# Performance work log

Hardware: AMD Instinct MI355X
Metric: run time of the kernel (lower is better)

## Reference

```python
import jax, jax.numpy as jnp
import numpy as np

DIM = 512
CHUNK = 64
LN_EPS = 1e-5


def setup_inputs() -> dict:
    key = jax.random.key(0)
    ks = jax.random.split(key, 9)
    B, S, D = 4, 4096, DIM
    x = jax.random.normal(ks[0], (B, S, D), dtype=jnp.float32)
    # Linear weights stored as [in, out] (equivalent to torch W.T)
    W_omega = jax.random.normal(ks[1], (D, D), dtype=jnp.float32) / np.sqrt(D)
    b_omega = jnp.zeros((D,), dtype=jnp.float32)
    log_scale = jnp.full((D,), np.log(0.1), dtype=jnp.float32)
    ln_gamma = jnp.ones((4 * D,), dtype=jnp.float32)
    ln_beta = jnp.zeros((4 * D,), dtype=jnp.float32)
    W1 = jax.random.normal(ks[2], (4 * D, 2 * D), dtype=jnp.float32) / np.sqrt(4 * D)
    b1 = jnp.zeros((2 * D,), dtype=jnp.float32)
    W2 = jax.random.normal(ks[3], (2 * D, D), dtype=jnp.float32) / np.sqrt(2 * D)
    b2 = jnp.zeros((D,), dtype=jnp.float32)
    return {"x": x, "W_omega": W_omega, "b_omega": b_omega, "log_scale": log_scale,
            "ln_gamma": ln_gamma, "ln_beta": ln_beta, "W1": W1, "b1": b1, "W2": W2, "b2": b2}


def reference(x, W_omega, b_omega, log_scale, ln_gamma, ln_beta, W1, b1, W2, b2):
    B, S, D = x.shape
    C = CHUNK
    # S chosen as multiple of C, so pad_len == 0 (matches torch no-pad branch)
    N = S // C
    omega = x @ W_omega + b_omega                      # [B,S,D]
    oc = omega.reshape(B, N, C, D)
    xc = x.reshape(B, N, C, D)
    pos = jnp.arange(1, C + 1, dtype=x.dtype)          # [C]
    pos_scale = (1.0 / jnp.sqrt(pos))[None, None, :, None]
    scale = jnp.exp(log_scale)
    phi = jnp.cumsum(oc * scale * pos_scale, axis=2)   # [B,N,C,D]
    cos_phi = jnp.cos(phi)
    sin_phi = jnp.sin(phi)
    cr = xc * cos_phi                                   # content modulated real
    ci = xc * sin_phi                                   # content modulated imag
    pos_norm = pos[None, None, :, None]
    mr = jnp.cumsum(cr, axis=2) / pos_norm              # memory real
    mi = jnp.cumsum(ci, axis=2) / pos_norm              # memory imag
    rr = mr * cos_phi + mi * sin_phi                    # retrieved real
    ri = mi * cos_phi - mr * sin_phi                    # retrieved imag
    ctx = jnp.concatenate([cr.reshape(B, S, D), ci.reshape(B, S, D),
                           rr.reshape(B, S, D), ri.reshape(B, S, D)], axis=-1)  # [B,S,4D]
    mu = jnp.mean(ctx, axis=-1, keepdims=True)
    var = jnp.mean((ctx - mu) ** 2, axis=-1, keepdims=True)
    h = (ctx - mu) / jnp.sqrt(var + LN_EPS) * ln_gamma + ln_beta
    h = h @ W1 + b1
    h = jax.nn.gelu(h, approximate=False)               # torch GELU default = exact erf
    out = h @ W2 + b2                                   # dropout is identity at eval
    return x + out
```

## Files before the change

### kernel.cpp

```cpp
#include <hip/hip_runtime.h>
#include <hip/hip_bf16.h>
#include <math.h>


typedef __bf16 bf16x8 __attribute__((ext_vector_type(8)));
typedef __bf16 bf16x4 __attribute__((ext_vector_type(4)));
typedef __bf16 bf16x2 __attribute__((ext_vector_type(2)));
typedef float  f32x4  __attribute__((ext_vector_type(4)));

typedef __attribute__((address_space(1))) void* gas_ptr;
typedef __attribute__((address_space(3))) void* las_ptr;

__device__ __forceinline__ void load_lds16(const void* g, void* l) {
    __builtin_amdgcn_global_load_lds((gas_ptr)g, (las_ptr)l, 16, 0, 0);
}

__device__ __forceinline__ void transpose_tile(const float* __restrict__ in,
                                               __bf16* __restrict__ out,
                                               int K, int N, int bx, int by,
                                               float (*tile)[33])
{
    const int tid = threadIdx.x;
    const int tx = tid & 31, ty = tid >> 5;
    const int n0 = bx * 32, k0 = by * 32;
    #pragma unroll
    for (int i = 0; i < 32; i += 8)
        tile[ty + i][tx] = in[(size_t)(k0 + ty + i) * N + n0 + tx];
    __syncthreads();
    #pragma unroll
    for (int i = 0; i < 32; i += 8)
        out[(size_t)(n0 + ty + i) * K + k0 + tx] = (__bf16)tile[tx][ty + i];
}

__global__ __launch_bounds__(256)
void prep_kernel(const float* __restrict__ x, __bf16* __restrict__ xb,
                 const float* __restrict__ W_omega, __bf16* __restrict__ womT,
                 const float* __restrict__ W1, __bf16* __restrict__ w1T,
                 const float* __restrict__ W2, __bf16* __restrict__ w2T)
{
    __shared__ float tile[32][33];
    const int bid = blockIdx.x;
    if (bid < 8192) {
        int i = bid * 256 + threadIdx.x;
        float4 v = ((const float4*)x)[i];
        bf16x4 o = { (__bf16)v.x, (__bf16)v.y, (__bf16)v.z, (__bf16)v.w };
        ((bf16x4*)xb)[i] = o;
    } else if (bid < 8448) {
        int t = bid - 8192;
        transpose_tile(W_omega, womT, 512, 512, t & 15, t >> 4, tile);
    } else if (bid < 10496) {
        int t = bid - 8448;
        transpose_tile(W1, w1T, 2048, 1024, t & 31, t >> 5, tile);
    } else {
        int t = bid - 10496;
        transpose_tile(W2, w2T, 1024, 512, t & 15, t >> 4, tile);
    }
}

template<int MODE>
__global__ __launch_bounds__(256)
void gemm_kernel(const __bf16* __restrict__ A, const __bf16* __restrict__ Bt,
                 const float* __restrict__ bias, const __bf16* __restrict__ resid,
                 void* __restrict__ out, int M, int N, int K)
{
    __shared__ __bf16 As[2][128 * 64];
    __shared__ __bf16 Bs[2][128 * 64];

    const int tid     = threadIdx.x;
    const int tiles_n = N >> 7;
    const int ln_tn   = __ffs(tiles_n) - 1;
    const int per_m   = (M >> 7) >> 3;

    const int xcd = blockIdx.x & 7;
    const int j   = blockIdx.x >> 3;
    const int tile_m = (xcd * per_m + (j >> ln_tn)) << 7;
    const int tile_n = (j & (tiles_n - 1)) << 7;

    const int wave = tid >> 6;
    const int lane = tid & 63;

    const int srow = lane >> 3;
    const int scol = ((lane & 7) ^ srow) << 3;

    const __bf16* Ags = A  + (size_t)(tile_m + wave * 32 + srow) * K + scol;
    const __bf16* Bgs = Bt + (size_t)(tile_n + wave * 32 + srow) * K + scol;

    const int m0 = (wave >> 1) << 6;
    const int n0 = (wave & 1) << 6;
    const int lr = lane & 15;
    const int q  = lane >> 4;
    const int l7 = lane & 7;
    const int fc0 = ((0 + q) ^ l7) << 3;
    const int fc1 = ((4 + q) ^ l7) << 3;

    f32x4 acc[4][4];
    #pragma unroll
    for (int i = 0; i < 4; ++i)
        #pragma unroll
        for (int jj = 0; jj < 4; ++jj)
            acc[i][jj] = (f32x4){0.f, 0.f, 0.f, 0.f};

    const int nIter = K >> 6;

    #pragma unroll
    for (int c = 0; c < 4; ++c) {
        load_lds16(Ags + (size_t)(c * 8) * K, &As[0][(wave * 32 + c * 8) * 64]);
        load_lds16(Bgs + (size_t)(c * 8) * K, &Bs[0][(wave * 32 + c * 8) * 64]);
    }

    for (int it = 0; it < nIter; ++it) {
        const int cur = it & 1;
        __syncthreads();
        if (it + 1 < nIter) {
            const int nk = (it + 1) << 6;
            #pragma unroll
            for (int c = 0; c < 4; ++c) {
                load_lds16(Ags + nk + (size_t)(c * 8) * K, &As[cur ^ 1][(wave * 32 + c * 8) * 64]);
                load_lds16(Bgs + nk + (size_t)(c * 8) * K, &Bs[cur ^ 1][(wave * 32 + c * 8) * 64]);
            }
        }

        const __bf16* as = As[cur];
        const __bf16* bs = Bs[cur];
        {
            bf16x8 af[4], bq[4];
            #pragma unroll
            for (int i = 0; i < 4; ++i)
                af[i] = *(const bf16x8*)&as[(m0 + i * 16 + lr) * 64 + fc0];
            #pragma unroll
            for (int jj = 0; jj < 4; ++jj)
                bq[jj] = *(const bf16x8*)&bs[(n0 + jj * 16 + lr) * 64 + fc0];
            #pragma unroll
            for (int i = 0; i < 4; ++i)
                #pragma unroll
                for (int jj = 0; jj < 4; ++jj)
                    acc[i][jj] = __builtin_amdgcn_mfma_f32_16x16x32_bf16(af[i], bq[jj], acc[i][jj], 0, 0, 0);
        }
        {
            bf16x8 af[4], bq[4];
            #pragma unroll
            for (int i = 0; i < 4; ++i)
                af[i] = *(const bf16x8*)&as[(m0 + i * 16 + lr) * 64 + fc1];
            #pragma unroll
            for (int jj = 0; jj < 4; ++jj)
                bq[jj] = *(const bf16x8*)&bs[(n0 + jj * 16 + lr) * 64 + fc1];
            #pragma unroll
            for (int i = 0; i < 4; ++i)
                #pragma unroll
                for (int jj = 0; jj < 4; ++jj)
                    acc[i][jj] = __builtin_amdgcn_mfma_f32_16x16x32_bf16(af[i], bq[jj], acc[i][jj], 0, 0, 0);
        }
    }

    const int orow0 = tile_m + m0 + (q << 2);
    const int ocol0 = tile_n + n0 + lr;
    #pragma unroll
    for (int i = 0; i < 4; ++i) {
        #pragma unroll
        for (int jj = 0; jj < 4; ++jj) {
            const int col = ocol0 + jj * 16;
            const float bv = bias[col];
            #pragma unroll
            for (int r = 0; r < 4; ++r) {
                const int row = orow0 + i * 16 + r;
                float v = acc[i][jj][r] + bv;
                size_t idx = (size_t)row * N + col;
                if (MODE == 0) {
                    ((__bf16*)out)[idx] = (__bf16)v;
                } else if (MODE == 1) {
                    float g = 0.5f * v * (1.0f + erff(v * 0.70710678118654752f));
                    ((__bf16*)out)[idx] = (__bf16)g;
                } else {
                    ((float*)out)[idx] = v + (float)resid[idx];
                }
            }
        }
    }
}

template<int MODE>
__global__ __launch_bounds__(512, 1)
void gemm256_kernel(const __bf16* __restrict__ A, const __bf16* __restrict__ Bt,
                    const float* __restrict__ bias, void* __restrict__ out,
                    int M, int N, int K)
{
    __shared__ __bf16 As[4][256 * 32];
    __shared__ __bf16 Bs[4][256 * 32];

    const int tid  = threadIdx.x;
    const int wv   = tid >> 6;
    const int lane = tid & 63;
    const int wm   = wv >> 2;
    const int wn   = wv & 3;

    const int tiles_n = N >> 8;
    const int ln_tn   = __ffs(tiles_n) - 1;
    const int per_m   = (M >> 8) >> 3;

    const int xcd = blockIdx.x & 7;
    const int j   = blockIdx.x >> 3;
    const int tile_m = (xcd * per_m + (j >> ln_tn)) << 8;
    const int tile_n = (j & (tiles_n - 1)) << 8;

    const int srow = 16 * wv + (lane >> 2);
    const int sig8 = (((lane & 3) ^ ((lane >> 3) & 3)) << 3);

    const __bf16* Ag = A  + (size_t)(tile_m + srow) * K + sig8;
    const __bf16* Bg = Bt + (size_t)(tile_n + srow) * K + sig8;
    const size_t rowK128 = (size_t)128 * K;
    const int lbase = wv * 512;

    const int lr    = lane & 15;
    const int q4    = lane >> 4;
    const int fslot = ((q4 ^ ((lane >> 1) & 3)) << 3);
    const int arow0 = wm * 128 + lr;
    const int brow0 = wn * 64 + lr;

    const unsigned ldsA0 = (unsigned)(size_t)(las_ptr)&As[0][0];
    const unsigned ldsB0 = (unsigned)(size_t)(las_ptr)&Bs[0][0];
    const unsigned asA = ldsA0 + (unsigned)((arow0 * 32 + fslot) << 1);
    const unsigned asB = ldsB0 + (unsigned)((brow0 * 32 + fslot) << 1);

    f32x4 acc[8][4];
    #pragma unroll
    for (int i = 0; i < 8; ++i)
        #pragma unroll
        for (int jj = 0; jj < 4; ++jj)
            acc[i][jj] = (f32x4){0.f, 0.f, 0.f, 0.f};

    const int NKS = K >> 5;

    auto stage = [&](int ks) {
        const int slot = ks & 3;
        const __bf16* ag = Ag + (ks << 5);
        const __bf16* bg = Bg + (ks << 5);
        load_lds16(ag,           &As[slot][lbase]);
        load_lds16(ag + rowK128, &As[slot][4096 + lbase]);
        load_lds16(bg,           &Bs[slot][lbase]);
        load_lds16(bg + rowK128, &Bs[slot][4096 + lbase]);
    };

    bf16x8 afA[8], bqA[4], afB[8], bqB[4];

#define DSR(d, a, o) asm volatile("ds_read_b128 %0, %1 offset:" o \
                                  : "=v"(d) : "v"(a))
#define SB __builtin_amdgcn_sched_barrier(0)
#define MM4(CAF, CBQ, I)                                                      \
    acc[I][0] = __builtin_amdgcn_mfma_f32_16x16x32_bf16(CAF[I], CBQ[0], acc[I][0], 0, 0, 0); \
    acc[I][1] = __builtin_amdgcn_mfma_f32_16x16x32_bf16(CAF[I], CBQ[1], acc[I][1], 0, 0, 0); \
    acc[I][2] = __builtin_amdgcn_mfma_f32_16x16x32_bf16(CAF[I], CBQ[2], acc[I][2], 0, 0, 0); \
    acc[I][3] = __builtin_amdgcn_mfma_f32_16x16x32_bf16(CAF[I], CBQ[3], acc[I][3], 0, 0, 0);

#define G256_READ(KS, NAF, NBQ)                                               \
    {                                                                         \
        const unsigned aA_ = asA + (unsigned)(((KS) & 3) << 14);              \
        const unsigned aB_ = asB + (unsigned)(((KS) & 3) << 14);              \
        DSR(NAF[0], aA_, "0");    DSR(NAF[1], aA_, "1024");                   \
        DSR(NAF[2], aA_, "2048"); DSR(NAF[3], aA_, "3072");                   \
        DSR(NAF[4], aA_, "4096"); DSR(NAF[5], aA_, "5120");                   \
        DSR(NAF[6], aA_, "6144"); DSR(NAF[7], aA_, "7168");                   \
        DSR(NBQ[0], aB_, "0");    DSR(NBQ[1], aB_, "1024");                   \
        DSR(NBQ[2], aB_, "2048"); DSR(NBQ[3], aB_, "3072");                   \
    }

#define G256_PHASE_FULL(KS, CAF, CBQ, NAF, NBQ)                               \
    {                                                                         \
        const int ks_ = (KS);                                                 \
        asm volatile("s_waitcnt vmcnt(8)" ::: "memory");                      \
        __builtin_amdgcn_s_barrier();                                         \
        asm volatile("" ::: "memory");                                        \
        const int slot_ = (ks_ + 4) & 3;                                      \
        const __bf16* ag_ = Ag + ((ks_ + 4) << 5);                            \
        const __bf16* bg_ = Bg + ((ks_ + 4) << 5);                            \
        const unsigned aA_ = asA + (unsigned)(((ks_ + 1) & 3) << 14);         \
        const unsigned aB_ = asB + (unsigned)(((ks_ + 1) & 3) << 14);         \
        __builtin_amdgcn_s_setprio(1);                                        \
        load_lds16(ag_,           &As[slot_][lbase]);                         \
        MM4(CAF, CBQ, 0) SB;                                                  \
        load_lds16(ag_ + rowK128, &As[slot_][4096 + lbase]);                  \
        MM4(CAF, CBQ, 1) SB;                                                  \
        load_lds16(bg_,           &Bs[slot_][lbase]);                         \
        MM4(CAF, CBQ, 2) SB;                                                  \
        load_lds16(bg_ + rowK128, &Bs[slot_][4096 + lbase]);                  \
        MM4(CAF, CBQ, 3) SB;                                                  \
        DSR(NAF[0], aA_, "0"); DSR(NAF[1], aA_, "1024");                      \
        DSR(NAF[2], aA_, "2048");                                             \
        MM4(CAF, CBQ, 4) SB;                                                  \
        DSR(NAF[3], aA_, "3072"); DSR(NAF[4], aA_, "4096");                   \
        DSR(NAF[5], aA_, "5120");                                             \
        MM4(CAF, CBQ, 5) SB;                                                  \
        DSR(NAF[6], aA_, "6144"); DSR(NAF[7], aA_, "7168");                   \
        DSR(NBQ[0], aB_, "0");                                                \
        MM4(CAF, CBQ, 6) SB;                                                  \
        DSR(NBQ[1], aB_, "1024"); DSR(NBQ[2], aB_, "2048");                   \
        DSR(NBQ[3], aB_, "3072");                                             \
        MM4(CAF, CBQ, 7)                                                      \
        __builtin_amdgcn_s_setprio(0);                                        \
        asm volatile("s_waitcnt lgkmcnt(0)" ::: "memory");                    \
        __builtin_amdgcn_sched_barrier(0);                                    \
    }

#define G256_PHASE_TAIL(KS, CAF, CBQ, NAF, NBQ)                               \
    {                                                                         \
        const int ks_ = (KS);                                                 \
        const int r_  = NKS - 1 - ks_;                                        \
        if (r_ >= 3)      asm volatile("s_waitcnt vmcnt(8)" ::: "memory");    \
        else if (r_ == 2) asm volatile("s_waitcnt vmcnt(4)" ::: "memory");    \
        else if (r_ == 1) asm volatile("s_waitcnt vmcnt(0)" ::: "memory");    \
        __builtin_amdgcn_s_barrier();                                         \
        asm volatile("" ::: "memory");                                        \
        if (ks_ + 4 < NKS) stage(ks_ + 4);                                    \
        if (ks_ + 1 < NKS) G256_READ(ks_ + 1, NAF, NBQ)                       \
        __builtin_amdgcn_s_setprio(1);                                        \
        _Pragma("unroll")                                                     \
        for (int i_ = 0; i_ < 8; ++i_)                                        \
            _Pragma("unroll")                                                 \
            for (int j_ = 0; j_ < 4; ++j_)                                    \
                acc[i_][j_] = __builtin_amdgcn_mfma_f32_16x16x32_bf16(        \
                    CAF[i_], CBQ[j_], acc[i_][j_], 0, 0, 0);                  \
        __builtin_amdgcn_s_setprio(0);                                        \
        asm volatile("s_waitcnt lgkmcnt(0)" ::: "memory");                    \
        __builtin_amdgcn_sched_barrier(0);                                    \
    }

    stage(0); stage(1); stage(2);
    asm volatile("s_waitcnt vmcnt(8)" ::: "memory");
    __builtin_amdgcn_s_barrier();
    asm volatile("" ::: "memory");
    stage(3);
    G256_READ(0, afA, bqA)
    asm volatile("s_waitcnt lgkmcnt(0)" ::: "memory");
    __builtin_amdgcn_sched_barrier(0);

    int ks = 0;
    for (; ks + 6 < NKS; ks += 2) {
        G256_PHASE_FULL(ks,     afA, bqA, afB, bqB)
        G256_PHASE_FULL(ks + 1, afB, bqB, afA, bqA)
    }
    for (; ks < NKS; ks += 2) {
        G256_PHASE_TAIL(ks,     afA, bqA, afB, bqB)
        G256_PHASE_TAIL(ks + 1, afB, bqB, afA, bqA)
    }

#undef G256_PHASE_FULL
#undef G256_PHASE_TAIL
#undef G256_READ
#undef MM4
#undef SB
#undef DSR

    const int orow0 = tile_m + wm * 128 + (q4 << 2);
    const int ocol0 = tile_n + wn * 64 + lr;
    #pragma unroll
    for (int i = 0; i < 8; ++i) {
        #pragma unroll
        for (int jj = 0; jj < 4; ++jj) {
            const int col = ocol0 + jj * 16;
            const float bv = bias[col];
            #pragma unroll
            for (int r = 0; r < 4; ++r) {
                const int row = orow0 + i * 16 + r;
                float v = acc[i][jj][r] + bv;
                if (MODE == 1) {
                    float g = 0.5f * v * (1.0f + erff(v * 0.70710678118654752f));
                    ((__bf16*)out)[(size_t)row * N + col] = (__bf16)g;
                } else {
                    ((__bf16*)out)[(size_t)row * N + col] = (__bf16)v;
                }
            }
        }
    }
}

__global__ __launch_bounds__(64)
void scan_ln_kernel(const __bf16* __restrict__ xb, const __bf16* __restrict__ omega,
                    const float* __restrict__ log_scale,
                    const float* __restrict__ gamma, const float* __restrict__ beta,
                    __bf16* __restrict__ ctx)
{
    const int chunk = blockIdx.x;
    const int lane  = threadIdx.x;
    const int d0    = lane << 3;
    const size_t base = (size_t)chunk * 64 * 512;

    float scale[8], g0[8], g1[8], g2[8], g3[8], e0[8], e1[8], e2[8], e3[8];
    #pragma unroll
    for (int u = 0; u < 8; ++u) {
        const int d = d0 + u;
        scale[u] = expf(log_scale[d]);
        g0[u] = gamma[d]; g1[u] = gamma[512 + d]; g2[u] = gamma[1024 + d]; g3[u] = gamma[1536 + d];
        e0[u] = beta[d];  e1[u] = beta[512 + d];  e2[u] = beta[1024 + d];  e3[u] = beta[1536 + d];
    }

    float phi[8], scr[8], sci[8];
    #pragma unroll
    for (int u = 0; u < 8; ++u) { phi[u] = 0.f; scr[u] = 0.f; sci[u] = 0.f; }

    bf16x8 om_n = *(const bf16x8*)&omega[base + d0];
    bf16x8 xv_n = *(const bf16x8*)&xb[base + d0];

    for (int c = 0; c < 64; ++c) {
        const bf16x8 omv = om_n;
        const bf16x8 xvv = xv_n;
        if (c < 63) {
            om_n = *(const bf16x8*)&omega[base + (size_t)(c + 1) * 512 + d0];
            xv_n = *(const bf16x8*)&xb[base + (size_t)(c + 1) * 512 + d0];
        }
        const float rsq = rsqrtf((float)(c + 1));
        const float inv = 1.0f / (float)(c + 1);

        float cr[8], ci[8], rr[8], ri[8];
        float s = 0.f, s2 = 0.f;
        #pragma unroll
        for (int u = 0; u < 8; ++u) {
            const float om = (float)omv[u];
            const float xv = (float)xvv[u];
            phi[u] += om * scale[u] * rsq;
            float sp, cp;
            __sincosf(phi[u], &sp, &cp);
            cr[u] = xv * cp; ci[u] = xv * sp;
            scr[u] += cr[u]; sci[u] += ci[u];
            const float mr = scr[u] * inv, mi = sci[u] * inv;
            rr[u] = mr * cp + mi * sp;
            ri[u] = mi * cp - mr * sp;
            s  += cr[u] + ci[u] + rr[u] + ri[u];
            s2 += cr[u]*cr[u] + ci[u]*ci[u] + rr[u]*rr[u] + ri[u]*ri[u];
        }
        #pragma unroll
        for (int o = 32; o > 0; o >>= 1) {
            s  += __shfl_xor(s, o);
            s2 += __shfl_xor(s2, o);
        }
        const float mu   = s * (1.0f / 2048.0f);
        const float var  = s2 * (1.0f / 2048.0f) - mu * mu;
        const float rstd = rsqrtf(var + 1e-5f);

        const size_t ob = ((size_t)chunk * 64 + c) * 2048;
        bf16x8 o0, o1, o2, o3;
        #pragma unroll
        for (int u = 0; u < 8; ++u) {
            o0[u] = (__bf16)(((cr[u] - mu) * rstd) * g0[u] + e0[u]);
            o1[u] = (__bf16)(((ci[u] - mu) * rstd) * g1[u] + e1[u]);
            o2[u] = (__bf16)(((rr[u] - mu) * rstd) * g2[u] + e2[u]);
            o3[u] = (__bf16)(((ri[u] - mu) * rstd) * g3[u] + e3[u]);
        }
        *(bf16x8*)&ctx[ob + d0]        = o0;
        *(bf16x8*)&ctx[ob + 512 + d0]  = o1;
        *(bf16x8*)&ctx[ob + 1024 + d0] = o2;
        *(bf16x8*)&ctx[ob + 1536 + d0] = o3;
    }
}

extern "C" void kernel_launch(void* const* d_in, const int* in_sizes, int n_in,
                              void* d_out, int out_size, void* d_ws, size_t ws_size,
                              hipStream_t stream)
{
    const float* x         = (const float*)d_in[0];
    const float* W_omega   = (const float*)d_in[1];
    const float* b_omega   = (const float*)d_in[2];
    const float* log_scale = (const float*)d_in[3];
    const float* ln_gamma  = (const float*)d_in[4];
    const float* ln_beta   = (const float*)d_in[5];
    const float* W1        = (const float*)d_in[6];
    const float* b1        = (const float*)d_in[7];
    const float* W2        = (const float*)d_in[8];
    const float* b2        = (const float*)d_in[9];
    float* out = (float*)d_out;

    char* ws = (char*)d_ws;
    __bf16* xb    = (__bf16*)(ws);
    __bf16* womT  = (__bf16*)(ws + 16777216);
    __bf16* w1T   = (__bf16*)(ws + 17301504);
    __bf16* w2T   = (__bf16*)(ws + 21495808);
    __bf16* omega = (__bf16*)(ws + 22544384);
    __bf16* hbuf  = (__bf16*)(ws + 22544384);
    __bf16* ctx   = (__bf16*)(ws + 56098816);

    prep_kernel<<<11008, 256, 0, stream>>>(x, xb, W_omega, womT, W1, w1T, W2, w2T);

    gemm_kernel<0><<<512, 256, 0, stream>>>(xb, womT, b_omega, nullptr, omega, 16384, 512, 512);

    scan_ln_kernel<<<256, 64, 0, stream>>>(xb, omega, log_scale, ln_gamma, ln_beta, ctx);

    gemm256_kernel<1><<<256, 512, 0, stream>>>(ctx, w1T, b1, hbuf, 16384, 1024, 2048);

    gemm_kernel<2><<<512, 256, 0, stream>>>(hbuf, w2T, b2, xb, out, 16384, 512, 1024);
}
```

Before: 296.7 us.

## Spread scan/LayerNorm kernel over four waves per chunk with LDS reduction

The scan+LayerNorm kernel now launches 256 threads per chunk instead of one wave, with each thread handling 2 feature columns instead of 8. Row statistics are reduced across the four waves through a double-buffered shared array and a __syncthreads per timestep. This raises parallelism for a kernel that had only 256 single-wave blocks on a large GPU, shortening each thread's serial chain of sincos work. In exchange it adds a block barrier per row and uses narrower 4-byte loads and stores.

```diff
diff --git a/kernel.cpp b/kernel.cpp
--- a/kernel.cpp
+++ b/kernel.cpp
@@ -372,47 +372,47 @@
     }
 }
 
-__global__ __launch_bounds__(64)
+__global__ __launch_bounds__(256)
 void scan_ln_kernel(const __bf16* __restrict__ xb, const __bf16* __restrict__ omega,
                     const float* __restrict__ log_scale,
                     const float* __restrict__ gamma, const float* __restrict__ beta,
                     __bf16* __restrict__ ctx)
 {
     const int chunk = blockIdx.x;
-    const int lane  = threadIdx.x;
-    const int d0    = lane << 3;
+    const int tid   = threadIdx.x;
+    const int lane  = tid & 63, wv = tid >> 6;
+    const int d0    = tid << 1;
     const size_t base = (size_t)chunk * 64 * 512;
 
-    float scale[8], g0[8], g1[8], g2[8], g3[8], e0[8], e1[8], e2[8], e3[8];
-    #pragma unroll
-    for (int u = 0; u < 8; ++u) {
+    float scale[2], g0[2], g1[2], g2[2], g3[2], e0[2], e1[2], e2[2], e3[2];
+    #pragma unroll
+    for (int u = 0; u < 2; ++u) {
         const int d = d0 + u;
         scale[u] = expf(log_scale[d]);
         g0[u] = gamma[d]; g1[u] = gamma[512 + d]; g2[u] = gamma[1024 + d]; g3[u] = gamma[1536 + d];
         e0[u] = beta[d];  e1[u] = beta[512 + d];  e2[u] = beta[1024 + d];  e3[u] = beta[1536 + d];
     }
 
-    float phi[8], scr[8], sci[8];
-    #pragma unroll
-    for (int u = 0; u < 8; ++u) { phi[u] = 0.f; scr[u] = 0.f; sci[u] = 0.f; }
-
-    bf16x8 om_n = *(const bf16x8*)&omega[base + d0];
-    bf16x8 xv_n = *(const bf16x8*)&xb[base + d0];
+    float phi[2] = {0.f, 0.f}, scr[2] = {0.f, 0.f}, sci[2] = {0.f, 0.f};
+    __shared__ float red[2][8];
+
+    bf16x2 om_n = *(const bf16x2*)&omega[base + d0];
+    bf16x2 xv_n = *(const bf16x2*)&xb[base + d0];
 
     for (int c = 0; c < 64; ++c) {
-        const bf16x8 omv = om_n;
-        const bf16x8 xvv = xv_n;
+        const bf16x2 omv = om_n;
+        const bf16x2 xvv = xv_n;
         if (c < 63) {
-            om_n = *(const bf16x8*)&omega[base + (size_t)(c + 1) * 512 + d0];
-            xv_n = *(const bf16x8*)&xb[base + (size_t)(c + 1) * 512 + d0];
+            om_n = *(const bf16x2*)&omega[base + (size_t)(c + 1) * 512 + d0];
+            xv_n = *(const bf16x2*)&xb[base + (size_t)(c + 1) * 512 + d0];
         }
         const float rsq = rsqrtf((float)(c + 1));
         const float inv = 1.0f / (float)(c + 1);
 
-        float cr[8], ci[8], rr[8], ri[8];
+        float cr[2], ci[2], rr[2], ri[2];
         float s = 0.f, s2 = 0.f;
         #pragma unroll
-        for (int u = 0; u < 8; ++u) {
+        for (int u = 0; u < 2; ++u) {
             const float om = (float)omv[u];
             const float xv = (float)xvv[u];
             phi[u] += om * scale[u] * rsq;
@@ -431,23 +431,27 @@
             s  += __shfl_xor(s, o);
             s2 += __shfl_xor(s2, o);
         }
-        const float mu   = s * (1.0f / 2048.0f);
-        const float var  = s2 * (1.0f / 2048.0f) - mu * mu;
+        if (lane == 0) { red[c & 1][wv] = s; red[c & 1][4 + wv] = s2; }
+        __syncthreads();
+        const float S  = red[c & 1][0] + red[c & 1][1] + red[c & 1][2] + red[c & 1][3];
+        const float S2 = red[c & 1][4] + red[c & 1][5] + red[c & 1][6] + red[c & 1][7];
+        const float mu   = S * (1.0f / 2048.0f);
+        const float var  = S2 * (1.0f / 2048.0f) - mu * mu;
         const float rstd = rsqrtf(var + 1e-5f);
 
         const size_t ob = ((size_t)chunk * 64 + c) * 2048;
-        bf16x8 o0, o1, o2, o3;
-        #pragma unroll
-        for (int u = 0; u < 8; ++u) {
+        bf16x2 o0, o1, o2, o3;
+        #pragma unroll
+        for (int u = 0; u < 2; ++u) {
             o0[u] = (__bf16)(((cr[u] - mu) * rstd) * g0[u] + e0[u]);
             o1[u] = (__bf16)(((ci[u] - mu) * rstd) * g1[u] + e1[u]);
             o2[u] = (__bf16)(((rr[u] - mu) * rstd) * g2[u] + e2[u]);
             o3[u] = (__bf16)(((ri[u] - mu) * rstd) * g3[u] + e3[u]);
         }
-        *(bf16x8*)&ctx[ob + d0]        = o0;
-        *(bf16x8*)&ctx[ob + 512 + d0]  = o1;
-        *(bf16x8*)&ctx[ob + 1024 + d0] = o2;
-        *(bf16x8*)&ctx[ob + 1536 + d0] = o3;
+        *(bf16x2*)&ctx[ob + d0]        = o0;
+        *(bf16x2*)&ctx[ob + 512 + d0]  = o1;
+        *(bf16x2*)&ctx[ob + 1024 + d0] = o2;
+        *(bf16x2*)&ctx[ob + 1536 + d0] = o3;
     }
 }
 
@@ -480,7 +484,7 @@
 
     gemm_kernel<0><<<512, 256, 0, stream>>>(xb, womT, b_omega, nullptr, omega, 16384, 512, 512);
 
-    scan_ln_kernel<<<256, 64, 0, stream>>>(xb, omega, log_scale, ln_gamma, ln_beta, ctx);
+    scan_ln_kernel<<<256, 256, 0, stream>>>(xb, omega, log_scale, ln_gamma, ln_beta, ctx);
 
     gemm256_kernel<1><<<256, 512, 0, stream>>>(ctx, w1T, b1, hbuf, 16384, 1024, 2048);
 
```

After: 263.8 us. 1.12x faster.

## Fuse chunked scan and layernorm into the first MLP GEMM kernel

Applied to the files above, without the earlier changes.

Removes the standalone scan_ln kernel and runs the per-chunk phase/memory scan plus layernorm at the start of the 256x256 GEMM kernel. Four waves per block compute the block's own 256 ctx rows, then a full waitcnt and barrier hand off to the GEMM main loop. This drops one kernel launch and the gap between stages. In exchange, each M-tile's scan is recomputed by all four N-tile blocks, so ctx is written redundantly, and half the waves sit idle during the scan. The GEMM output moves to a separate workspace region so it no longer aliases the omega buffer that the fused kernel still reads.

```diff
diff --git a/kernel.cpp b/kernel.cpp
--- a/kernel.cpp
+++ b/kernel.cpp
@@ -178,11 +178,13 @@
     }
 }
 
-template<int MODE>
 __global__ __launch_bounds__(512, 1)
-void gemm256_kernel(const __bf16* __restrict__ A, const __bf16* __restrict__ Bt,
-                    const float* __restrict__ bias, void* __restrict__ out,
-                    int M, int N, int K)
+void scan_gemm_kernel(const __bf16* __restrict__ xbp, const __bf16* __restrict__ omega,
+                      const float* __restrict__ log_scale,
+                      const float* __restrict__ gamma, const float* __restrict__ beta,
+                      __bf16* ctx,
+                      const __bf16* __restrict__ Bt, const float* __restrict__ bias,
+                      __bf16* __restrict__ out, int M, int N, int K)
 {
     __shared__ __bf16 As[4][256 * 32];
     __shared__ __bf16 Bs[4][256 * 32];
@@ -201,6 +203,82 @@
     const int j   = blockIdx.x >> 3;
     const int tile_m = (xcd * per_m + (j >> ln_tn)) << 8;
     const int tile_n = (j & (tiles_n - 1)) << 8;
+
+    if (wv < 4) {
+        const int chunk = (tile_m >> 6) + wv;
+        const int d0    = lane << 3;
+        const size_t sbase = (size_t)chunk * 64 * 512;
+
+        float scale[8], g0[8], g1[8], g2[8], g3[8], e0[8], e1[8], e2[8], e3[8];
+        #pragma unroll
+        for (int u = 0; u < 8; ++u) {
+            const int d = d0 + u;
+            scale[u] = expf(log_scale[d]);
+            g0[u] = gamma[d]; g1[u] = gamma[512 + d]; g2[u] = gamma[1024 + d]; g3[u] = gamma[1536 + d];
+            e0[u] = beta[d];  e1[u] = beta[512 + d];  e2[u] = beta[1024 + d];  e3[u] = beta[1536 + d];
+        }
+        float phi[8], scr[8], sci[8];
+        #pragma unroll
+        for (int u = 0; u < 8; ++u) { phi[u] = 0.f; scr[u] = 0.f; sci[u] = 0.f; }
+
+        bf16x8 om_n = *(const bf16x8*)&omega[sbase + d0];
+        bf16x8 xv_n = *(const bf16x8*)&xbp[sbase + d0];
+
+        for (int c = 0; c < 64; ++c) {
+            const bf16x8 omv = om_n;
+            const bf16x8 xvv = xv_n;
+            if (c < 63) {
+                om_n = *(const bf16x8*)&omega[sbase + (size_t)(c + 1) * 512 + d0];
+                xv_n = *(const bf16x8*)&xbp[sbase + (size_t)(c + 1) * 512 + d0];
+            }
+            const float rsq = rsqrtf((float)(c + 1));
+            const float inv = 1.0f / (float)(c + 1);
+
+            float cr[8], ci[8], rr[8], ri[8];
+            float s = 0.f, s2 = 0.f;
+            #pragma unroll
+            for (int u = 0; u < 8; ++u) {
+                const float om = (float)omv[u];
+                const float xv = (float)xvv[u];
+                phi[u] += om * scale[u] * rsq;
+                float sp, cp;
+                __sincosf(phi[u], &sp, &cp);
+                cr[u] = xv * cp; ci[u] = xv * sp;
+                scr[u] += cr[u]; sci[u] += ci[u];
+                const float mr = scr[u] * inv, mi = sci[u] * inv;
+                rr[u] = mr * cp + mi * sp;
+                ri[u] = mi * cp - mr * sp;
+                s  += cr[u] + ci[u] + rr[u] + ri[u];
+                s2 += cr[u]*cr[u] + ci[u]*ci[u] + rr[u]*rr[u] + ri[u]*ri[u];
+            }
+            #pragma unroll
+            for (int o = 32; o > 0; o >>= 1) {
+                s  += __shfl_xor(s, o);
+                s2 += __shfl_xor(s2, o);
+            }
+            const float mu   = s * (1.0f / 2048.0f);
+            const float var  = s2 * (1.0f / 2048.0f) - mu * mu;
+            const float rstd = rsqrtf(var + 1e-5f);
+
+            const size_t ob = ((size_t)chunk * 64 + c) * 2048;
+            bf16x8 o0, o1, o2, o3;
+            #pragma unroll
+            for (int u = 0; u < 8; ++u) {
+                o0[u] = (__bf16)(((cr[u] - mu) * rstd) * g0[u] + e0[u]);
+                o1[u] = (__bf16)(((ci[u] - mu) * rstd) * g1[u] + e1[u]);
+                o2[u] = (__bf16)(((rr[u] - mu) * rstd) * g2[u] + e2[u]);
+                o3[u] = (__bf16)(((ri[u] - mu) * rstd) * g3[u] + e3[u]);
+            }
+            *(bf16x8*)&ctx[ob + d0]        = o0;
+            *(bf16x8*)&ctx[ob + 512 + d0]  = o1;
+            *(bf16x8*)&ctx[ob + 1024 + d0] = o2;
+            *(bf16x8*)&ctx[ob + 1536 + d0] = o3;
+        }
+    }
+    asm volatile("s_waitcnt vmcnt(0)" ::: "memory");
+    __syncthreads();
+
+    const __bf16* A = ctx;
 
     const int srow = 16 * wv + (lane >> 2);
     const int sig8 = (((lane & 3) ^ ((lane >> 3) & 3)) << 3);
@@ -361,93 +439,10 @@
             for (int r = 0; r < 4; ++r) {
                 const int row = orow0 + i * 16 + r;
                 float v = acc[i][jj][r] + bv;
-                if (MODE == 1) {
-                    float g = 0.5f * v * (1.0f + erff(v * 0.70710678118654752f));
-                    ((__bf16*)out)[(size_t)row * N + col] = (__bf16)g;
-                } else {
-                    ((__bf16*)out)[(size_t)row * N + col] = (__bf16)v;
-                }
-            }
-        }
-    }
-}
-
-__global__ __launch_bounds__(64)
-void scan_ln_kernel(const __bf16* __restrict__ xb, const __bf16* __restrict__ omega,
-                    const float* __restrict__ log_scale,
-                    const float* __restrict__ gamma, const float* __restrict__ beta,
-                    __bf16* __restrict__ ctx)
-{
-    const int chunk = blockIdx.x;
-    const int lane  = threadIdx.x;
-    const int d0    = lane << 3;
-    const size_t base = (size_t)chunk * 64 * 512;
-
-    float scale[8], g0[8], g1[8], g2[8], g3[8], e0[8], e1[8], e2[8], e3[8];
-    #pragma unroll
-    for (int u = 0; u < 8; ++u) {
-        const int d = d0 + u;
-        scale[u] = expf(log_scale[d]);
-        g0[u] = gamma[d]; g1[u] = gamma[512 + d]; g2[u] = gamma[1024 + d]; g3[u] = gamma[1536 + d];
-        e0[u] = beta[d];  e1[u] = beta[512 + d];  e2[u] = beta[1024 + d];  e3[u] = beta[1536 + d];
-    }
-
-    float phi[8], scr[8], sci[8];
-    #pragma unroll
-    for (int u = 0; u < 8; ++u) { phi[u] = 0.f; scr[u] = 0.f; sci[u] = 0.f; }
-
-    bf16x8 om_n = *(const bf16x8*)&omega[base + d0];
-    bf16x8 xv_n = *(const bf16x8*)&xb[base + d0];
-
-    for (int c = 0; c < 64; ++c) {
-        const bf16x8 omv = om_n;
-        const bf16x8 xvv = xv_n;
-        if (c < 63) {
-            om_n = *(const bf16x8*)&omega[base + (size_t)(c + 1) * 512 + d0];
-            xv_n = *(const bf16x8*)&xb[base + (size_t)(c + 1) * 512 + d0];
-        }
-        const float rsq = rsqrtf((float)(c + 1));
-        const float inv = 1.0f / (float)(c + 1);
-
-        float cr[8], ci[8], rr[8], ri[8];
-        float s = 0.f, s2 = 0.f;
-        #pragma unroll
-        for (int u = 0; u < 8; ++u) {
-            const float om = (float)omv[u];
-            const float xv = (float)xvv[u];
-            phi[u] += om * scale[u] * rsq;
-            float sp, cp;
-            __sincosf(phi[u], &sp, &cp);
-            cr[u] = xv * cp; ci[u] = xv * sp;
-            scr[u] += cr[u]; sci[u] += ci[u];
-            const float mr = scr[u] * inv, mi = sci[u] * inv;
-            rr[u] = mr * cp + mi * sp;
-            ri[u] = mi * cp - mr * sp;
-            s  += cr[u] + ci[u] + rr[u] + ri[u];
-            s2 += cr[u]*cr[u] + ci[u]*ci[u] + rr[u]*rr[u] + ri[u]*ri[u];
-        }
-        #pragma unroll
-        for (int o = 32; o > 0; o >>= 1) {
-            s  += __shfl_xor(s, o);
-            s2 += __shfl_xor(s2, o);
-        }
-        const float mu   = s * (1.0f / 2048.0f);
-        const float var  = s2 * (1.0f / 2048.0f) - mu * mu;
-        const float rstd = rsqrtf(var + 1e-5f);
-
-        const size_t ob = ((size_t)chunk * 64 + c) * 2048;
-        bf16x8 o0, o1, o2, o3;
-        #pragma unroll
-        for (int u = 0; u < 8; ++u) {
-            o0[u] = (__bf16)(((cr[u] - mu) * rstd) * g0[u] + e0[u]);
-            o1[u] = (__bf16)(((ci[u] - mu) * rstd) * g1[u] + e1[u]);
-            o2[u] = (__bf16)(((rr[u] - mu) * rstd) * g2[u] + e2[u]);
-            o3[u] = (__bf16)(((ri[u] - mu) * rstd) * g3[u] + e3[u]);
-        }
-        *(bf16x8*)&ctx[ob + d0]        = o0;
-        *(bf16x8*)&ctx[ob + 512 + d0]  = o1;
-        *(bf16x8*)&ctx[ob + 1024 + d0] = o2;
-        *(bf16x8*)&ctx[ob + 1536 + d0] = o3;
+                float g = 0.5f * v * (1.0f + erff(v * 0.70710678118654752f));
+                out[(size_t)row * N + col] = (__bf16)g;
+            }
+        }
     }
 }
 
@@ -480,9 +475,12 @@
 
     gemm_kernel<0><<<512, 256, 0, stream>>>(xb, womT, b_omega, nullptr, omega, 16384, 512, 512);
 
-    scan_ln_kernel<<<256, 64, 0, stream>>>(xb, omega, log_scale, ln_gamma, ln_beta, ctx);
-
-    gemm256_kernel<1><<<256, 512, 0, stream>>>(ctx, w1T, b1, hbuf, 16384, 1024, 2048);
-
-    gemm_kernel<2><<<512, 256, 0, stream>>>(hbuf, w2T, b2, xb, out, 16384, 512, 1024);
-}
+    {
+        __bf16* hsafe = (__bf16*)(ws + 123207680);
+        scan_gemm_kernel<<<256, 512, 0, stream>>>(xb, omega, log_scale, ln_gamma,
+                                                  ln_beta, ctx, w1T, b1, hsafe,
+                                                  16384, 1024, 2048);
+
+        gemm_kernel<2><<<512, 256, 0, stream>>>(hsafe, w2T, b2, xb, out, 16384, 512, 1024);
+    }
+}
```

Result: faster. 277.2 us (-6.6%).
